# Performance work log

Measured on AMD Instinct MI355X. Metric: run time of the kernel, lower is better.

## Reference

```python
import jax, jax.numpy as jnp
import numpy as np

NUM_HEADS, KEY_DIM, BLOCK, HALO = 8, 64, 8, 4
KV_KERNEL = BLOCK + 2 * HALO  # 16
EMB = NUM_HEADS * KEY_DIM     # 512


def setup_inputs() -> dict:
    key = jax.random.key(0)
    k = jax.random.split(key, 6)
    stddev = KEY_DIM ** -0.5
    return {
        "x": jax.random.normal(k[0], (8, 64, 64, 512), jnp.float32),
        "wq": jax.random.normal(k[1], (512, EMB), jnp.float32) * 0.02,
        "wkv": jax.random.normal(k[2], (512, 2 * EMB), jnp.float32) * 0.02,
        "wout": jax.random.normal(k[3], (EMB, EMB), jnp.float32) * 0.02,
        "pos_w": jax.random.normal(k[4], (KEY_DIM, 2 * KV_KERNEL - 1), jnp.float32) * stddev,
        "pos_h": jax.random.normal(k[5], (KEY_DIM, 2 * KV_KERNEL - 1), jnp.float32) * stddev,
    }


def rel_to_abs(rel):
    # rel: [B, N, hh, ww, 2*pos_dim-1] -> [B, N, hh, ww, pos_dim]
    b, n, hh, ww, dim = rel.shape
    pos_dim = (dim + 1) // 2
    gap = pos_dim - ww
    flat = rel.reshape(b, n, hh, ww * dim)[:, :, :, ww - 1:-1]
    return flat.reshape(b, n, hh, ww, 2 * (pos_dim - 1))[:, :, :, :, gap:pos_dim + gap]


def halo_forward(x, wq, wkv, wout, pos_w, pos_h):
    B, H, W, C = x.shape
    h, w = H // BLOCK, W // BLOCK
    K = KV_KERNEL
    scale = 1.0 / jnp.sqrt(jnp.asarray(KEY_DIM, x.dtype))

    # Query: [B, hd, h, w, block^2, key_dim]
    q = (x @ wq) * scale
    q = q.reshape(B, h, BLOCK, w, BLOCK, NUM_HEADS, KEY_DIM)
    attn_q = q.transpose(0, 5, 1, 3, 2, 4, 6).reshape(B, NUM_HEADS, h, w, BLOCK * BLOCK, KEY_DIM)

    # Overlapping halo KV windows (im2col-style gather, like tf.image.extract_patches)
    kv = x @ wkv
    kv_p = jnp.pad(kv, ((0, 0), (HALO, HALO), (HALO, HALO), (0, 0)))
    idx_h = jnp.arange(h)[:, None] * BLOCK + jnp.arange(K)[None, :]  # [h, K]
    idx_w = jnp.arange(w)[:, None] * BLOCK + jnp.arange(K)[None, :]  # [w, K]
    patches = kv_p[:, idx_h][:, :, :, idx_w]          # [B, h, K, w, K, 2*EMB]
    patches = patches.transpose(0, 1, 3, 2, 4, 5)     # [B, h, w, K, K, 2*EMB]
    patches = patches.reshape(B, h, w, K * K, NUM_HEADS, 2 * KEY_DIM)
    patches = patches.transpose(0, 4, 1, 2, 3, 5)     # [B, hd, h, w, K^2, 2*key_dim]
    key_t, val = patches[..., :KEY_DIM], patches[..., KEY_DIM:]

    scores = jnp.einsum('bnhwqc,bnhwkc->bnhwqk', attn_q, key_t)  # [B,hd,h,w,bq,bk]

    # Relative position logits (width + height), query already carries qk_scale
    pos_q = attn_q.reshape(B, NUM_HEADS * h * w, BLOCK, BLOCK, KEY_DIM)
    rel_w = rel_to_abs(pos_q @ pos_w)                                      # [B,N,hb,wb,K]
    rel_h = rel_to_abs(pos_q.transpose(0, 1, 3, 2, 4) @ pos_h)
    rel_h = rel_h.transpose(0, 1, 3, 2, 4)                                 # [B,N,hb,wb,K]
    pos = rel_w[..., None, :] + rel_h[..., :, None]                        # [B,N,hb,wb,Kh,Kw]
    pos = pos.reshape(B, NUM_HEADS, h, w, BLOCK * BLOCK, K * K)

    attn = jax.nn.softmax(scores + pos, axis=-1)
    out = jnp.einsum('bnhwqk,bnhwkc->bnhwqc', attn, val)
    out = out.reshape(B, NUM_HEADS, h, w, BLOCK, BLOCK, KEY_DIM)
    out = out.transpose(0, 2, 4, 3, 5, 1, 6).reshape(B, H, W, EMB)
    return out @ wout


def reference(x, wq, wkv, wout, pos_w, pos_h):
    return halo_forward(x, wq, wkv, wout, pos_w, pos_h)
```

## Files before the change

### kernel.cpp

```cpp
#include <hip/hip_runtime.h>
#include <hip/hip_fp16.h>
#include <math.h>

typedef _Float16 f16x8 __attribute__((ext_vector_type(8)));
typedef _Float16 f16x4 __attribute__((ext_vector_type(4)));
typedef float    f32x4 __attribute__((ext_vector_type(4)));

#define M_TOT 32768
#define VROW  4608

__device__ __forceinline__ void gload16(const void* g, void* l) {
    __builtin_amdgcn_global_load_lds(
        (const __attribute__((address_space(1))) unsigned int*)g,
        (__attribute__((address_space(3))) unsigned int*)l, 16, 0, 0);
}

__global__ __launch_bounds__(256) void conv_x(const float* __restrict__ x,
                                              __half* __restrict__ y) {
    const size_t i = ((size_t)blockIdx.x * 256 + threadIdx.x) * 8;
    float4 a = *(const float4*)&x[i];
    float4 b = *(const float4*)&x[i + 4];
    __half2 h[4];
    h[0] = __floats2half2_rn(a.x, a.y);
    h[1] = __floats2half2_rn(a.z, a.w);
    h[2] = __floats2half2_rn(b.x, b.y);
    h[3] = __floats2half2_rn(b.z, b.w);
    *(float4*)&y[i] = *(float4*)h;
}

__global__ __launch_bounds__(256) void conv_w(const float* __restrict__ wq,
                                              const float* __restrict__ wkv,
                                              const float* __restrict__ wout,
                                              __half* __restrict__ wT,
                                              __half* __restrict__ woT) {
    const int id = blockIdx.x * 256 + threadIdx.x;
    const int nr = id >> 9, k = id & 511;
    if (nr < 512) {
        wT[(size_t)nr * 512 + k]  = __float2half(wq[k * 512 + nr] * 0.125f);
    } else if (nr < 1536) {
        wT[(size_t)nr * 512 + k]  = __float2half(wkv[k * 1024 + (nr - 512)]);
    } else {
        woT[(size_t)(nr - 1536) * 512 + k] = __float2half(wout[k * 512 + (nr - 1536)]);
    }
}

__global__ __launch_bounds__(256) void vborder(__half* __restrict__ vTp) {
    const int id = blockIdx.x * 256 + threadIdx.x;
    const int row = id >> 7, rem = id & 127;
    const int y = rem >> 1, side = rem & 1;
    f16x4 z = {(_Float16)0.f, (_Float16)0.f, (_Float16)0.f, (_Float16)0.f};
    *(f16x4*)(vTp + (size_t)row * VROW + y * 72 + side * 68) = z;
}

template <int MODE, int NBN>
__global__ __launch_bounds__(256) void mfma_gemm(
    const __half* __restrict__ A, const __half* __restrict__ Bt,
    __half* __restrict__ q16, __half* __restrict__ k16, __half* __restrict__ vTp,
    float* __restrict__ outf)
{
    __shared__ _Float16 As[128 * 32];
    __shared__ _Float16 Bs[128 * 32];

    const int t = threadIdx.x;
    const int l = t & 63, w = t >> 6;
    const int wr = w >> 1, wc = w & 1;

    const int bid = blockIdx.x;
    const int xcd = bid & 7, loc = bid >> 3;
    const int bm  = xcd * 32 + (loc & 31);
    const int bn  = loc >> 5;

    f32x4 zero = {0.f, 0.f, 0.f, 0.f};
    f32x4 acc[4][4];
    #pragma unroll
    for (int i = 0; i < 4; ++i)
        #pragma unroll
        for (int j = 0; j < 4; ++j) acc[i][j] = zero;

    const int srow = w * 32 + (l >> 2);
    const int sch  = (l & 3) * 8;
    const size_t abase = (size_t)(bm * 128 + srow) * 512 + sch;
    const size_t bbase = (size_t)(bn * 128 + srow) * 512 + sch;
    _Float16* ldsA0 = &As[(w * 2 + 0) * 512];
    _Float16* ldsA1 = &As[(w * 2 + 1) * 512];
    _Float16* ldsB0 = &Bs[(w * 2 + 0) * 512];
    _Float16* ldsB1 = &Bs[(w * 2 + 1) * 512];

    const int lr = l & 15, lk = (l >> 4) * 8;

    for (int k0 = 0; k0 < 512; k0 += 32) {
        gload16(A  + abase + k0,            ldsA0);
        gload16(A  + abase + 16 * 512 + k0, ldsA1);
        gload16(Bt + bbase + k0,            ldsB0);
        gload16(Bt + bbase + 16 * 512 + k0, ldsB1);
        __syncthreads();

        f16x8 af[4], bf[4];
        #pragma unroll
        for (int i = 0; i < 4; ++i)
            af[i] = *(const f16x8*)&As[(wr * 64 + i * 16 + lr) * 32 + lk];
        #pragma unroll
        for (int j = 0; j < 4; ++j)
            bf[j] = *(const f16x8*)&Bs[(wc * 64 + j * 16 + lr) * 32 + lk];
        #pragma unroll
        for (int i = 0; i < 4; ++i)
            #pragma unroll
            for (int j = 0; j < 4; ++j)
                acc[i][j] = __builtin_amdgcn_mfma_f32_16x16x32_f16(af[i], bf[j], acc[i][j], 0, 0, 0);
        __syncthreads();
    }

    const int lq = l >> 4;
    #pragma unroll
    for (int i = 0; i < 4; ++i) {
        #pragma unroll
        for (int j = 0; j < 4; ++j) {
            const int row0 = bm * 128 + wr * 64 + i * 16 + lq * 4;
            const int col  = bn * 128 + wc * 64 + j * 16 + lr;
            if (MODE == 1) {
                #pragma unroll
                for (int r = 0; r < 4; ++r)
                    outf[(size_t)(row0 + r) * 512 + col] = acc[i][j][r];
            } else if (bn < 4) {
                #pragma unroll
                for (int r = 0; r < 4; ++r)
                    q16[(size_t)(row0 + r) * 512 + col] = __float2half(acc[i][j][r]);
            } else if (wc == 0) {
                const int head = bn - 4, d2 = j * 16 + lr;
                #pragma unroll
                for (int r = 0; r < 4; ++r)
                    k16[(size_t)(row0 + r) * 512 + head * 64 + d2] = __float2half(acc[i][j][r]);
            } else {
                const int head = bn - 4, d2 = j * 16 + lr;
                const int bb = row0 >> 12, pix = row0 & 4095;
                const int py = pix >> 6, px = pix & 63;
                f16x4 pv;
                #pragma unroll
                for (int r = 0; r < 4; ++r) pv[r] = (_Float16)acc[i][j][r];
                *(f16x4*)(vTp + ((size_t)((bb * 8 + head) * 64 + d2)) * VROW + py * 72 + px + 4) = pv;
            }
        }
    }
}

__global__ __launch_bounds__(256, 3) void halo_attn(
    const __half* __restrict__ qbuf, const __half* __restrict__ kbuf,
    const __half* __restrict__ vTp,
    const float* __restrict__ posw, const float* __restrict__ posh,
    const __half* __restrict__ zp,
    __half* __restrict__ obuf)
{
    __shared__ __align__(16) char KP[64 * 528];
    __shared__ __align__(16) char PTRW[17408];
    __shared__ float red[4][64];
    __shared__ float red2[4][64];

    float (*RWT)[68] = (float(*)[68])PTRW;
    float (*RHT)[68] = (float(*)[68])(PTRW + 8704);

    const int hw = blockIdx.x;
    const int wg = (hw & 7) * 512 + (hw >> 3);
    const int wb = wg & 7, hb = (wg >> 3) & 7, n = (wg >> 6) & 7, b = wg >> 9;
    const int t = threadIdx.x;
    const int l = t & 63, g = t >> 6;
    const int hi = l >> 4, c15 = l & 15;

    #pragma unroll
    for (int it = 0; it < 8; ++it) {
        const int cid = it * 256 + t;
        const int S = cid * 16;
        const int row = S >> 7;
        const int d0h = (((S & 127) >> 4) ^ (row & 7)) * 8;
        const int ky = hb * 8 - 4 + (row >> 4);
        const int kx = wb * 8 - 4 + (row & 15);
        const bool ok = ((unsigned)ky < 64u) && ((unsigned)kx < 64u);
        const __half* src = ok ? (kbuf + ((size_t)((b * 64 + ky) * 64 + kx)) * 512 + n * 64 + d0h)
                               : zp;
        gload16(src, KP + (it * 256 + g * 64) * 16);
    }

    f16x8 vfrag[8];
    {
        const __half* vrow = vTp + ((size_t)((b * 8 + n) * 64 + g * 16 + c15)) * VROW;
        const int xoff = wb * 8 + (hi & 1) * 8;
        #pragma unroll
        for (int kc = 0; kc < 8; ++kc) {
            const int ki = kc * 2 + (hi >> 1);
            const int y = hb * 8 - 4 + ki;
            const __half* p = ((unsigned)y < 64u) ? (vrow + y * 72 + xoff) : zp;
            vfrag[kc] = *(const f16x8*)p;
        }
    }

    for (int j5 = t; j5 < 4096; j5 += 256) {
        const int tb = j5 >> 11, idx = (j5 >> 6) & 31, d = j5 & 63;
        const float* src = tb ? posh : posw;
        const float v = (idx < 31) ? src[d * 31 + idx] : 0.f;
        *(__half*)(PTRW + tb * 4096 + ((idx * 128 + d * 2) ^ ((idx & 7) << 4))) = __float2half(v);
    }

    f16x8 qreg[4][2];
    #pragma unroll
    for (int qf = 0; qf < 4; ++qf) {
        const int q = qf * 16 + c15;
        const size_t pix = (size_t)((b * 64 + hb * 8 + (q >> 3)) * 64 + wb * 8 + (q & 7));
        #pragma unroll
        for (int dc = 0; dc < 2; ++dc)
            qreg[qf][dc] = *(const f16x8*)(qbuf + pix * 512 + n * 64 + dc * 32 + hi * 8);
    }
    __syncthreads();

    f32x4 accp[4];
    #pragma unroll
    for (int qf = 0; qf < 4; ++qf) accp[qf] = (f32x4){0.f, 0.f, 0.f, 0.f};
    {
        const int tb = g >> 1, ih = g & 1;
        const char* base = PTRW + tb * 4096;
        const int row = ih * 16 + c15;
        #pragma unroll
        for (int dc = 0; dc < 2; ++dc) {
            const int off = (row * 128 + dc * 64 + hi * 16) ^ ((row & 7) << 4);
            f16x8 a = *(const f16x8*)(base + off);
            #pragma unroll
            for (int qf = 0; qf < 4; ++qf)
                accp[qf] = __builtin_amdgcn_mfma_f32_16x16x32_f16(a, qreg[qf][dc], accp[qf], 0, 0, 0);
        }
    }
    __syncthreads();

    {
        const int tb = g >> 1, ih = g & 1;
        float (*dst)[68] = tb ? RHT : RWT;
        #pragma unroll
        for (int qf = 0; qf < 4; ++qf)
            #pragma unroll
            for (int r = 0; r < 4; ++r)
                dst[ih * 16 + hi * 4 + r][qf * 16 + c15] = accp[qf][r];
    }
    __syncthreads();

    f32x4 accs[4][4];
    #pragma unroll
    for (int kf = 0; kf < 4; ++kf)
        #pragma unroll
        for (int qf = 0; qf < 4; ++qf) accs[kf][qf] = (f32x4){0.f, 0.f, 0.f, 0.f};

    #pragma unroll
    for (int kf = 0; kf < 4; ++kf) {
        const int row = g * 64 + kf * 16 + c15;
        #pragma unroll
        for (int dc = 0; dc < 2; ++dc) {
            const int off = (row * 128 + dc * 64 + hi * 16) ^ ((row & 7) << 4);
            f16x8 a = *(const f16x8*)(KP + off);
            #pragma unroll
            for (int qf = 0; qf < 4; ++qf)
                accs[kf][qf] = __builtin_amdgcn_mfma_f32_16x16x32_f16(a, qreg[qf][dc], accs[kf][qf], 0, 0, 0);
        }
    }

    float mq[4];
    #pragma unroll
    for (int qf = 0; qf < 4; ++qf) {
        const int q = qf * 16 + c15;
        const int qj = q & 7, qi = q >> 3;
        float pa[4], pb[4];
        #pragma unroll
        for (int r = 0; r < 4; ++r)  pa[r] = RWT[hi * 4 + r - qj + 15][q];
        #pragma unroll
        for (int kf = 0; kf < 4; ++kf) pb[kf] = RHT[g * 4 + kf - qi + 15][q];
        float mm = -1e30f;
        #pragma unroll
        for (int kf = 0; kf < 4; ++kf)
            #pragma unroll
            for (int r = 0; r < 4; ++r) {
                const float s = accs[kf][qf][r] + pa[r] + pb[kf];
                accs[kf][qf][r] = s;
                mm = fmaxf(mm, s);
            }
        mm = fmaxf(mm, __shfl_xor(mm, 16));
        mm = fmaxf(mm, __shfl_xor(mm, 32));
        mq[qf] = mm;
    }
    if (l < 16) {
        #pragma unroll
        for (int qf = 0; qf < 4; ++qf) red[g][qf * 16 + l] = mq[qf];
    }
    __syncthreads();

    float sums[4];
    #pragma unroll
    for (int qf = 0; qf < 4; ++qf) {
        const int q = qf * 16 + c15;
        const float mfull = fmaxf(fmaxf(red[0][q], red[1][q]), fmaxf(red[2][q], red[3][q]));
        float ss = 0.f;
        #pragma unroll
        for (int kf = 0; kf < 4; ++kf)
            #pragma unroll
            for (int r = 0; r < 4; ++r) {
                const float p = __expf(accs[kf][qf][r] - mfull);
                accs[kf][qf][r] = p;
                ss += p;
            }
        ss += __shfl_xor(ss, 16);
        ss += __shfl_xor(ss, 32);
        sums[qf] = ss;
        #pragma unroll
        for (int kf = 0; kf < 4; ++kf) {
            __half2 h01 = __floats2half2_rn(accs[kf][qf][0], accs[kf][qf][1]);
            __half2 h23 = __floats2half2_rn(accs[kf][qf][2], accs[kf][qf][3]);
            uint2 wv;
            wv.x = *(unsigned*)&h01;
            wv.y = *(unsigned*)&h23;
            const int koff = (g * 64 + kf * 16 + hi * 4) * 2;
            *(uint2*)(KP + q * 528 + (koff ^ ((q & 7) << 4))) = wv;
        }
    }
    if (l < 16) {
        #pragma unroll
        for (int qf = 0; qf < 4; ++qf) red2[g][qf * 16 + l] = sums[qf];
    }
    __syncthreads();

    f32x4 acco[4];
    #pragma unroll
    for (int qf = 0; qf < 4; ++qf) acco[qf] = (f32x4){0.f, 0.f, 0.f, 0.f};
    #pragma unroll
    for (int kc = 0; kc < 8; ++kc) {
        const f16x8 bf = vfrag[kc];
        const int roff = (kc * 64 + hi * 16) ^ ((c15 & 7) << 4);
        #pragma unroll
        for (int qf = 0; qf < 4; ++qf) {
            const f16x8 af = *(const f16x8*)(KP + (qf * 16 + c15) * 528 + roff);
            acco[qf] = __builtin_amdgcn_mfma_f32_16x16x32_f16(af, bf, acco[qf], 0, 0, 0);
        }
    }

    #pragma unroll
    for (int qf = 0; qf < 4; ++qf) {
        #pragma unroll
        for (int r = 0; r < 4; ++r) {
            const int q = qf * 16 + hi * 4 + r;
            const float den = red2[0][q] + red2[1][q] + red2[2][q] + red2[3][q];
            const float v = acco[qf][r] / den;
            const size_t pix = (size_t)((b * 64 + hb * 8 + (q >> 3)) * 64 + wb * 8 + (q & 7));
            obuf[pix * 512 + n * 64 + g * 16 + c15] = __float2half(v);
        }
    }
}

extern "C" void kernel_launch(void* const* d_in, const int* in_sizes, int n_in,
                              void* d_out, int out_size, void* d_ws, size_t ws_size,
                              hipStream_t stream)
{
    const float* x    = (const float*)d_in[0];
    const float* wq   = (const float*)d_in[1];
    const float* wkv  = (const float*)d_in[2];
    const float* wout = (const float*)d_in[3];
    const float* posw = (const float*)d_in[4];
    const float* posh = (const float*)d_in[5];
    float* out = (float*)d_out;

    const size_t NPIX = (size_t)M_TOT * 512;
    const size_t NVTP = (size_t)64 * 64 * VROW;
    __half* x16 = (__half*)d_ws;
    __half* wT  = x16 + NPIX;
    __half* woT = wT + (size_t)1536 * 512;
    __half* q16 = woT + (size_t)512 * 512;
    __half* k16 = q16 + NPIX;
    __half* vTp = k16 + NPIX;
    __half* o16 = vTp + NVTP;
    __half* zp  = o16 + NPIX;

    hipMemsetAsync(zp, 0, 256, stream);

    conv_x<<<(M_TOT * 512) / (256 * 8), 256, 0, stream>>>(x, x16);
    conv_w<<<(2048 * 512) / 256, 256, 0, stream>>>(wq, wkv, wout, wT, woT);
    vborder<<<2048, 256, 0, stream>>>(vTp);

    mfma_gemm<0, 12><<<3072, 256, 0, stream>>>(x16, wT, q16, k16, vTp, nullptr);

    halo_attn<<<4096, 256, 0, stream>>>(q16, k16, vTp, posw, posh, zp, o16);

    mfma_gemm<1, 4><<<1024, 256, 0, stream>>>(o16, woT, nullptr, nullptr, nullptr, out);
}
```

Before: 231.4 us.

## Restructure halo attention so each wave owns 16 queries with register softmax

The attention kernel is reorganised so each wave handles 16 query pixels across all 256 keys. K and V fragments are loaded straight from global memory into registers instead of staging K in LDS, and the cross-wave max/sum reductions and most barriers are dropped. Position-embedding conversion moves into a small separate prep kernel, and P·V uses 16x16x16 MFMAs fed from the register-held probabilities. LDS use shrinks, allowing higher occupancy (launch bound 4), at the cost of more redundant global loads of K/V per wave and higher register pressure.

```diff
diff --git a/kernel.cpp b/kernel.cpp
--- a/kernel.cpp
+++ b/kernel.cpp
@@ -13,6 +13,10 @@
     __builtin_amdgcn_global_load_lds(
         (const __attribute__((address_space(1))) unsigned int*)g,
         (__attribute__((address_space(3))) unsigned int*)l, 16, 0, 0);
+}
+
+__device__ __forceinline__ f32x4 mfma32(f16x8 a, f16x8 b, f32x4 c) {
+    return __builtin_amdgcn_mfma_f32_16x16x32_f16(a, b, c, 0, 0, 0);
 }
 
 __global__ __launch_bounds__(256) void conv_x(const float* __restrict__ x,
@@ -44,6 +48,15 @@
     }
 }
 
+__global__ __launch_bounds__(256) void pos_prep(const float* __restrict__ posw,
+                                                const float* __restrict__ posh,
+                                                __half* __restrict__ posT) {
+    const int id = blockIdx.x * 256 + threadIdx.x;
+    const int tb = id >> 11, idx = (id >> 6) & 31, d = id & 63;
+    const float* src = tb ? posh : posw;
+    posT[id] = __float2half((idx < 31) ? src[d * 31 + idx] : 0.f);
+}
+
 __global__ __launch_bounds__(256) void vborder(__half* __restrict__ vTp) {
     const int id = blockIdx.x * 256 + threadIdx.x;
     const int row = id >> 7, rem = id & 127;
@@ -106,7 +119,7 @@
         for (int i = 0; i < 4; ++i)
             #pragma unroll
             for (int j = 0; j < 4; ++j)
-                acc[i][j] = __builtin_amdgcn_mfma_f32_16x16x32_f16(af[i], bf[j], acc[i][j], 0, 0, 0);
+                acc[i][j] = mfma32(af[i], bf[j], acc[i][j]);
         __syncthreads();
     }
 
@@ -143,20 +156,12 @@
     }
 }
 
-__global__ __launch_bounds__(256, 3) void halo_attn(
+__global__ __launch_bounds__(256, 4) void halo_attn(
     const __half* __restrict__ qbuf, const __half* __restrict__ kbuf,
-    const __half* __restrict__ vTp,
-    const float* __restrict__ posw, const float* __restrict__ posh,
-    const __half* __restrict__ zp,
-    __half* __restrict__ obuf)
+    const __half* __restrict__ vTp, const __half* __restrict__ posT,
+    const __half* __restrict__ zp, __half* __restrict__ obuf)
 {
-    __shared__ __align__(16) char KP[64 * 528];
-    __shared__ __align__(16) char PTRW[17408];
-    __shared__ float red[4][64];
-    __shared__ float red2[4][64];
-
-    float (*RWT)[68] = (float(*)[68])PTRW;
-    float (*RHT)[68] = (float(*)[68])(PTRW + 8704);
+    __shared__ float POS[4][2][32][17];
 
     const int hw = blockIdx.x;
     const int wg = (hw & 7) * 512 + (hw >> 3);
@@ -165,185 +170,123 @@
     const int l = t & 63, g = t >> 6;
     const int hi = l >> 4, c15 = l & 15;
 
-    #pragma unroll
-    for (int it = 0; it < 8; ++it) {
-        const int cid = it * 256 + t;
-        const int S = cid * 16;
-        const int row = S >> 7;
-        const int d0h = (((S & 127) >> 4) ^ (row & 7)) * 8;
-        const int ky = hb * 8 - 4 + (row >> 4);
-        const int kx = wb * 8 - 4 + (row & 15);
-        const bool ok = ((unsigned)ky < 64u) && ((unsigned)kx < 64u);
-        const __half* src = ok ? (kbuf + ((size_t)((b * 64 + ky) * 64 + kx)) * 512 + n * 64 + d0h)
-                               : zp;
-        gload16(src, KP + (it * 256 + g * 64) * 16);
-    }
-
-    f16x8 vfrag[8];
+    const int q  = g * 16 + c15;
+    const int qi = q >> 3, qj = q & 7;
+
+    f16x8 qreg[2];
     {
-        const __half* vrow = vTp + ((size_t)((b * 8 + n) * 64 + g * 16 + c15)) * VROW;
-        const int xoff = wb * 8 + (hi & 1) * 8;
-        #pragma unroll
-        for (int kc = 0; kc < 8; ++kc) {
-            const int ki = kc * 2 + (hi >> 1);
-            const int y = hb * 8 - 4 + ki;
-            const __half* p = ((unsigned)y < 64u) ? (vrow + y * 72 + xoff) : zp;
-            vfrag[kc] = *(const f16x8*)p;
-        }
-    }
-
-    for (int j5 = t; j5 < 4096; j5 += 256) {
-        const int tb = j5 >> 11, idx = (j5 >> 6) & 31, d = j5 & 63;
-        const float* src = tb ? posh : posw;
-        const float v = (idx < 31) ? src[d * 31 + idx] : 0.f;
-        *(__half*)(PTRW + tb * 4096 + ((idx * 128 + d * 2) ^ ((idx & 7) << 4))) = __float2half(v);
-    }
-
-    f16x8 qreg[4][2];
-    #pragma unroll
-    for (int qf = 0; qf < 4; ++qf) {
-        const int q = qf * 16 + c15;
-        const size_t pix = (size_t)((b * 64 + hb * 8 + (q >> 3)) * 64 + wb * 8 + (q & 7));
-        #pragma unroll
-        for (int dc = 0; dc < 2; ++dc)
-            qreg[qf][dc] = *(const f16x8*)(qbuf + pix * 512 + n * 64 + dc * 32 + hi * 8);
-    }
-    __syncthreads();
-
-    f32x4 accp[4];
-    #pragma unroll
-    for (int qf = 0; qf < 4; ++qf) accp[qf] = (f32x4){0.f, 0.f, 0.f, 0.f};
-    {
-        const int tb = g >> 1, ih = g & 1;
-        const char* base = PTRW + tb * 4096;
-        const int row = ih * 16 + c15;
-        #pragma unroll
-        for (int dc = 0; dc < 2; ++dc) {
-            const int off = (row * 128 + dc * 64 + hi * 16) ^ ((row & 7) << 4);
-            f16x8 a = *(const f16x8*)(base + off);
+        const size_t pix = (size_t)((b * 64 + hb * 8 + qi) * 64 + wb * 8 + qj);
+        qreg[0] = *(const f16x8*)(qbuf + pix * 512 + n * 64 + hi * 8);
+        qreg[1] = *(const f16x8*)(qbuf + pix * 512 + n * 64 + 32 + hi * 8);
+    }
+
+    #pragma unroll
+    for (int tb = 0; tb < 2; ++tb) {
+        #pragma unroll
+        for (int ih = 0; ih < 2; ++ih) {
+            f32x4 accp = {0.f, 0.f, 0.f, 0.f};
             #pragma unroll
-            for (int qf = 0; qf < 4; ++qf)
-                accp[qf] = __builtin_amdgcn_mfma_f32_16x16x32_f16(a, qreg[qf][dc], accp[qf], 0, 0, 0);
-        }
-    }
-    __syncthreads();
-
-    {
-        const int tb = g >> 1, ih = g & 1;
-        float (*dst)[68] = tb ? RHT : RWT;
-        #pragma unroll
-        for (int qf = 0; qf < 4; ++qf)
+            for (int dc = 0; dc < 2; ++dc) {
+                const f16x8 a = *(const f16x8*)(posT + tb * 2048 + (ih * 16 + c15) * 64 + dc * 32 + hi * 8);
+                accp = mfma32(a, qreg[dc], accp);
+            }
             #pragma unroll
             for (int r = 0; r < 4; ++r)
-                dst[ih * 16 + hi * 4 + r][qf * 16 + c15] = accp[qf][r];
-    }
-    __syncthreads();
-
-    f32x4 accs[4][4];
-    #pragma unroll
-    for (int kf = 0; kf < 4; ++kf)
-        #pragma unroll
-        for (int qf = 0; qf < 4; ++qf) accs[kf][qf] = (f32x4){0.f, 0.f, 0.f, 0.f};
-
-    #pragma unroll
-    for (int kf = 0; kf < 4; ++kf) {
-        const int row = g * 64 + kf * 16 + c15;
-        #pragma unroll
-        for (int dc = 0; dc < 2; ++dc) {
-            const int off = (row * 128 + dc * 64 + hi * 16) ^ ((row & 7) << 4);
-            f16x8 a = *(const f16x8*)(KP + off);
+                POS[g][tb][ih * 16 + hi * 4 + r][c15] = accp[r];
+        }
+    }
+
+    f32x4 accs[16];
+    #pragma unroll
+    for (int kf = 0; kf < 16; ++kf) accs[kf] = (f32x4){0.f, 0.f, 0.f, 0.f};
+
+    {
+        const int kxv = wb * 8 - 4 + c15;
+        const bool okx = (unsigned)kxv < 64u;
+        #pragma unroll
+        for (int kf = 0; kf < 16; ++kf) {
+            const int ky = hb * 8 - 4 + kf;
+            const bool ok = okx && ((unsigned)ky < 64u);
+            const __half* kp = ok ? (kbuf + ((size_t)((b * 64 + ky) * 64 + kxv)) * 512 + n * 64) : zp;
+            const f16x8 a0 = *(const f16x8*)(kp + hi * 8);
+            const f16x8 a1 = *(const f16x8*)(kp + 32 + hi * 8);
+            accs[kf] = mfma32(a0, qreg[0], accs[kf]);
+            accs[kf] = mfma32(a1, qreg[1], accs[kf]);
+        }
+    }
+
+    float pav[4];
+    #pragma unroll
+    for (int r = 0; r < 4; ++r) pav[r] = POS[g][0][hi * 4 + r - qj + 15][c15];
+    float mm = -1e30f;
+    #pragma unroll
+    for (int kf = 0; kf < 16; ++kf) {
+        const float pb = POS[g][1][kf - qi + 15][c15];
+        #pragma unroll
+        for (int r = 0; r < 4; ++r) {
+            const float s = accs[kf][r] + pav[r] + pb;
+            accs[kf][r] = s;
+            mm = fmaxf(mm, s);
+        }
+    }
+    mm = fmaxf(mm, __shfl_xor(mm, 16));
+    mm = fmaxf(mm, __shfl_xor(mm, 32));
+
+    float ss = 0.f;
+    #pragma unroll
+    for (int kf = 0; kf < 16; ++kf)
+        #pragma unroll
+        for (int r = 0; r < 4; ++r) {
+            const float p = __expf(accs[kf][r] - mm);
+            accs[kf][r] = p;
+            ss += p;
+        }
+    ss += __shfl_xor(ss, 16);
+    ss += __shfl_xor(ss, 32);
+    const float inv = 1.f / ss;
+
+    f16x4 afP[16];
+    #pragma unroll
+    for (int kf = 0; kf < 16; ++kf) {
+        __half2 h01 = __floats2half2_rn(accs[kf][0] * inv, accs[kf][1] * inv);
+        __half2 h23 = __floats2half2_rn(accs[kf][2] * inv, accs[kf][3] * inv);
+        uint2 u;
+        u.x = *(unsigned*)&h01;
+        u.y = *(unsigned*)&h23;
+        __builtin_memcpy(&afP[kf], &u, 8);
+    }
+
+    f32x4 acco[4];
+    #pragma unroll
+    for (int nf = 0; nf < 4; ++nf) acco[nf] = (f32x4){0.f, 0.f, 0.f, 0.f};
+    {
+        const __half* vb = vTp + ((size_t)((b * 8 + n) * 64)) * VROW;
+        const int xv = wb * 8 + hi * 4;
+        const __half* vrow[4];
+        #pragma unroll
+        for (int nf = 0; nf < 4; ++nf)
+            vrow[nf] = vb + (size_t)(nf * 16 + c15) * VROW + xv;
+        #pragma unroll
+        for (int kc = 0; kc < 16; ++kc) {
+            const int y = hb * 8 - 4 + kc;
+            const bool oky = (unsigned)y < 64u;
             #pragma unroll
-            for (int qf = 0; qf < 4; ++qf)
-                accs[kf][qf] = __builtin_amdgcn_mfma_f32_16x16x32_f16(a, qreg[qf][dc], accs[kf][qf], 0, 0, 0);
-        }
-    }
-
-    float mq[4];
-    #pragma unroll
-    for (int qf = 0; qf < 4; ++qf) {
-        const int q = qf * 16 + c15;
-        const int qj = q & 7, qi = q >> 3;
-        float pa[4], pb[4];
-        #pragma unroll
-        for (int r = 0; r < 4; ++r)  pa[r] = RWT[hi * 4 + r - qj + 15][q];
-        #pragma unroll
-        for (int kf = 0; kf < 4; ++kf) pb[kf] = RHT[g * 4 + kf - qi + 15][q];
-        float mm = -1e30f;
-        #pragma unroll
-        for (int kf = 0; kf < 4; ++kf)
-            #pragma unroll
-            for (int r = 0; r < 4; ++r) {
-                const float s = accs[kf][qf][r] + pa[r] + pb[kf];
-                accs[kf][qf][r] = s;
-                mm = fmaxf(mm, s);
+            for (int nf = 0; nf < 4; ++nf) {
+                const __half* vp = oky ? (vrow[nf] + y * 72) : zp;
+                f16x4 bf;
+                __builtin_memcpy(&bf, vp, 8);
+                acco[nf] = __builtin_amdgcn_mfma_f32_16x16x16f16(afP[kc], bf, acco[nf], 0, 0, 0);
             }
-        mm = fmaxf(mm, __shfl_xor(mm, 16));
-        mm = fmaxf(mm, __shfl_xor(mm, 32));
-        mq[qf] = mm;
-    }
-    if (l < 16) {
-        #pragma unroll
-        for (int qf = 0; qf < 4; ++qf) red[g][qf * 16 + l] = mq[qf];
-    }
-    __syncthreads();
-
-    float sums[4];
-    #pragma unroll
-    for (int qf = 0; qf < 4; ++qf) {
-        const int q = qf * 16 + c15;
-        const float mfull = fmaxf(fmaxf(red[0][q], red[1][q]), fmaxf(red[2][q], red[3][q]));
-        float ss = 0.f;
-        #pragma unroll
-        for (int kf = 0; kf < 4; ++kf)
-            #pragma unroll
-            for (int r = 0; r < 4; ++r) {
-                const float p = __expf(accs[kf][qf][r] - mfull);
-                accs[kf][qf][r] = p;
-                ss += p;
-            }
-        ss += __shfl_xor(ss, 16);
-        ss += __shfl_xor(ss, 32);
-        sums[qf] = ss;
-        #pragma unroll
-        for (int kf = 0; kf < 4; ++kf) {
-            __half2 h01 = __floats2half2_rn(accs[kf][qf][0], accs[kf][qf][1]);
-            __half2 h23 = __floats2half2_rn(accs[kf][qf][2], accs[kf][qf][3]);
-            uint2 wv;
-            wv.x = *(unsigned*)&h01;
-            wv.y = *(unsigned*)&h23;
-            const int koff = (g * 64 + kf * 16 + hi * 4) * 2;
-            *(uint2*)(KP + q * 528 + (koff ^ ((q & 7) << 4))) = wv;
-        }
-    }
-    if (l < 16) {
-        #pragma unroll
-        for (int qf = 0; qf < 4; ++qf) red2[g][qf * 16 + l] = sums[qf];
-    }
-    __syncthreads();
-
-    f32x4 acco[4];
-    #pragma unroll
-    for (int qf = 0; qf < 4; ++qf) acco[qf] = (f32x4){0.f, 0.f, 0.f, 0.f};
-    #pragma unroll
-    for (int kc = 0; kc < 8; ++kc) {
-        const f16x8 bf = vfrag[kc];
-        const int roff = (kc * 64 + hi * 16) ^ ((c15 & 7) << 4);
-        #pragma unroll
-        for (int qf = 0; qf < 4; ++qf) {
-            const f16x8 af = *(const f16x8*)(KP + (qf * 16 + c15) * 528 + roff);
-            acco[qf] = __builtin_amdgcn_mfma_f32_16x16x32_f16(af, bf, acco[qf], 0, 0, 0);
-        }
-    }
-
-    #pragma unroll
-    for (int qf = 0; qf < 4; ++qf) {
+        }
+    }
+
+    #pragma unroll
+    for (int nf = 0; nf < 4; ++nf) {
         #pragma unroll
         for (int r = 0; r < 4; ++r) {
-            const int q = qf * 16 + hi * 4 + r;
-            const float den = red2[0][q] + red2[1][q] + red2[2][q] + red2[3][q];
-            const float v = acco[qf][r] / den;
-            const size_t pix = (size_t)((b * 64 + hb * 8 + (q >> 3)) * 64 + wb * 8 + (q & 7));
-            obuf[pix * 512 + n * 64 + g * 16 + c15] = __float2half(v);
+            const int qq = g * 16 + hi * 4 + r;
+            const size_t pix = (size_t)((b * 64 + hb * 8 + (qq >> 3)) * 64 + wb * 8 + (qq & 7));
+            obuf[pix * 512 + n * 64 + nf * 16 + c15] = __float2half(acco[nf][r]);
         }
     }
 }
@@ -362,24 +305,26 @@
 
     const size_t NPIX = (size_t)M_TOT * 512;
     const size_t NVTP = (size_t)64 * 64 * VROW;
-    __half* x16 = (__half*)d_ws;
-    __half* wT  = x16 + NPIX;
-    __half* woT = wT + (size_t)1536 * 512;
-    __half* q16 = woT + (size_t)512 * 512;
-    __half* k16 = q16 + NPIX;
-    __half* vTp = k16 + NPIX;
-    __half* o16 = vTp + NVTP;
-    __half* zp  = o16 + NPIX;
+    __half* x16  = (__half*)d_ws;
+    __half* wT   = x16 + NPIX;
+    __half* woT  = wT + (size_t)1536 * 512;
+    __half* q16  = woT + (size_t)512 * 512;
+    __half* k16  = q16 + NPIX;
+    __half* vTp  = k16 + NPIX;
+    __half* o16  = vTp + NVTP;
+    __half* zp   = o16 + NPIX;
+    __half* posT = zp + 128;
 
     hipMemsetAsync(zp, 0, 256, stream);
 
     conv_x<<<(M_TOT * 512) / (256 * 8), 256, 0, stream>>>(x, x16);
     conv_w<<<(2048 * 512) / 256, 256, 0, stream>>>(wq, wkv, wout, wT, woT);
+    pos_prep<<<16, 256, 0, stream>>>(posw, posh, posT);
     vborder<<<2048, 256, 0, stream>>>(vTp);
 
     mfma_gemm<0, 12><<<3072, 256, 0, stream>>>(x16, wT, q16, k16, vTp, nullptr);
 
-    halo_attn<<<4096, 256, 0, stream>>>(q16, k16, vTp, posw, posh, zp, o16);
+    halo_attn<<<4096, 256, 0, stream>>>(q16, k16, vTp, posT, zp, o16);
 
     mfma_gemm<1, 4><<<1024, 256, 0, stream>>>(o16, woT, nullptr, nullptr, nullptr, out);
 }
```

New measurement: 332.1 us. +43.5%, slower.
